# Optimization experiments

Measured on AMD Instinct MI355X. Metric: run time of the kernel, lower is better.

## Reference

```python
import jax, jax.numpy as jnp
import numpy as np

L1, L2, B = 512, 512, 2
D1, D2, BN = 256, 256, 256
NEG = jnp.float32(-1e12)


def setup_inputs() -> dict:
    key = jax.random.key(0)
    ks = jax.random.split(key, 8)
    s = 0.05
    return {
        "ctx_1": jax.random.normal(ks[0], (L1, B, D1), jnp.float32),
        "ctx_2": jax.random.normal(ks[1], (L2, B, D2), jnp.float32),
        "ctx_1_mask": jnp.ones((L1, B), jnp.float32),
        "ctx_2_mask": jnp.ones((L2, B), jnp.float32),
        # mlp_hid: Conv2d(D1+D2 -> BN, 1x1) with bias
        "Wh": jax.random.normal(ks[2], (D1 + D2, BN), jnp.float32) * s,
        "bh": jnp.zeros((BN,), jnp.float32),
        # mlp_out: Conv2d(BN -> 1, 1x1), bias=False (mlp_bias default)
        "wo": jax.random.normal(ks[3], (BN,), jnp.float32) * s,
        # project_1_to_2 / project_2_to_1: Linear(D1+D2 -> BN) with bias
        "W12": jax.random.normal(ks[4], (D2 + D1, BN), jnp.float32) * s,
        "b12": jnp.zeros((BN,), jnp.float32),
        "W21": jax.random.normal(ks[5], (D1 + D2, BN), jnp.float32) * s,
        "b21": jnp.zeros((BN,), jnp.float32),
    }


def reference(ctx_1, ctx_2, ctx_1_mask, ctx_2_mask, Wh, bh, wo, W12, b12, W21, b21):
    d1 = ctx_1.shape[-1]
    # 1x1 conv on cat([b_ctx_1, b_ctx_2]) == sum of two independent projections
    Wh1, Wh2 = Wh[:d1], Wh[d1:]
    p1 = jnp.einsum('lbd,dk->blk', ctx_1, Wh1)            # (B, L1, K)
    p2 = jnp.einsum('mbd,dk->bmk', ctx_2, Wh2)            # (B, L2, K)
    hidden = jnp.tanh(p1[:, :, None, :] + p2[:, None, :, :] + bh)  # (B, L1, L2, K)
    affinity = jnp.einsum('blmk,k->blm', hidden, wo)      # (B, L1, L2)
    # masked in both directions
    affinity = affinity + (1.0 - ctx_1_mask.T)[:, :, None] * NEG
    affinity = affinity + (1.0 - ctx_2_mask.T)[:, None, :] * NEG
    # 1 -> 2 direction: softmax over L2
    dist_1_to_2 = jax.nn.softmax(affinity, axis=2)        # (B, L1, L2)
    context_1_to_2 = jnp.einsum('lbd,blm->mbd', ctx_1, dist_1_to_2)  # (L2, B, D1)
    seq_1_to_2 = jnp.tanh(jnp.concatenate([ctx_2, context_1_to_2], axis=-1) @ W12 + b12)
    # 2 -> 1 direction: softmax over L1 (then contracted over L2, as in the torch code)
    dist_2_to_1 = jax.nn.softmax(affinity, axis=1)        # (B, L1, L2)
    context_2_to_1 = jnp.einsum('mbd,blm->lbd', ctx_2, dist_2_to_1)  # (L1, B, D2)
    seq_2_to_1 = jnp.tanh(jnp.concatenate([ctx_1, context_2_to_1], axis=-1) @ W21 + b21)
    return (seq_2_to_1, seq_1_to_2)
```

## Files before the change

### kernel.cpp

```cpp
#include <hip/hip_runtime.h>


#define NEGC (-1e12f)
#define TWO_LOG2E 2.8853900817779268f
#define LOG2E 1.4426950408889634f
#define N2LOG2E (-2.8853900817779268f)

typedef __attribute__((ext_vector_type(8))) short bf16x8;
typedef __attribute__((ext_vector_type(4))) float f32x4;

__device__ __forceinline__ short f2bf(float x)
{
    union { float f; unsigned u; } v; v.f = x;
    unsigned r = (v.u + 0x7FFFu + ((v.u >> 16) & 1u)) >> 16;
    return (short)r;
}

__global__ __launch_bounds__(256) void k_proj(
    const float* __restrict__ ctx1, const float* __restrict__ ctx2,
    const float* __restrict__ Wh, const float* __restrict__ bh,
    const float* __restrict__ W12, const float* __restrict__ b12,
    const float* __restrict__ W21, const float* __restrict__ b21,
    const float* __restrict__ mask1, const float* __restrict__ mask2,
    float* __restrict__ E1, float* __restrict__ E2,
    float* __restrict__ P12, float* __restrict__ U1,
    float* __restrict__ P21, float* __restrict__ U2,
    float* __restrict__ p1, float* __restrict__ p2,
    float* __restrict__ S1, float* __restrict__ S2)
{
    const int t  = threadIdx.x;
    const int g  = blockIdx.z;
    const int r0 = blockIdx.x * 64;
    const int n0 = blockIdx.y * 64;

    const float* A; const float* W; const float* bias; int expm; float* outp;
    switch (g) {
      case 0:  A=ctx1; W=Wh;        bias=bh;   expm=1; outp=E1;  break;
      case 1:  A=ctx2; W=Wh+65536;  bias=0;    expm=1; outp=E2;  break;
      case 2:  A=ctx2; W=W12;       bias=b12;  expm=0; outp=P12; break;
      case 3:  A=ctx1; W=W12+65536; bias=0;    expm=0; outp=U1;  break;
      case 4:  A=ctx1; W=W21;       bias=b21;  expm=0; outp=P21; break;
      default: A=ctx2; W=W21+65536; bias=0;    expm=0; outp=U2;  break;
    }

    if (g == 0 && blockIdx.x == 0 && blockIdx.y == 0) {
        for (int idx = t; idx < 1024; idx += 256) {
            int row = idx >> 1, b = idx & 1;
            p1[b * 512 + row] = __builtin_amdgcn_exp2f(LOG2E * (1.f - mask1[idx]) * NEGC);
            p2[b * 512 + row] = __builtin_amdgcn_exp2f(LOG2E * (1.f - mask2[idx]) * NEGC);
            S1[b * 512 + row] = 0.f;
            S2[b * 512 + row] = 0.f;
        }
    }

    __shared__ __align__(16) short Abf[64 * 136];
    __shared__ __align__(16) short Bbf[64 * 136];

    const int w    = t >> 6;
    const int lane = t & 63;
    const int quad = lane >> 4;
    const int lr   = lane & 15;

    f32x4 acc[4] = {};

    for (int kc = 0; kc < 256; kc += 128) {
        #pragma unroll
        for (int i = 0; i < 8; ++i) {
            int slot = i * 256 + t;
            int r = slot >> 5, kq = (slot & 31) << 2;
            float4 v = *(const float4*)(A + (r0 + r) * 256 + kc + kq);
            short4 s; s.x = f2bf(v.x); s.y = f2bf(v.y); s.z = f2bf(v.z); s.w = f2bf(v.w);
            *(short4*)(Abf + r * 136 + kq) = s;
        }
        #pragma unroll
        for (int i = 0; i < 8; ++i) {
            int slot = i * 256 + t;
            int bk = slot >> 4, bn4 = (slot & 15) << 2;
            float4 v = *(const float4*)(W + (kc + bk) * 256 + n0 + bn4);
            Bbf[(bn4 + 0) * 136 + bk] = f2bf(v.x);
            Bbf[(bn4 + 1) * 136 + bk] = f2bf(v.y);
            Bbf[(bn4 + 2) * 136 + bk] = f2bf(v.z);
            Bbf[(bn4 + 3) * 136 + bk] = f2bf(v.w);
        }
        __syncthreads();
        #pragma unroll
        for (int s = 0; s < 4; ++s) {
            const int kb = s * 32 + quad * 8;
            bf16x8 a = *(const bf16x8*)(Abf + (w * 16 + lr) * 136 + kb);
            #pragma unroll
            for (int nc = 0; nc < 4; ++nc) {
                bf16x8 b = *(const bf16x8*)(Bbf + (nc * 16 + lr) * 136 + kb);
                acc[nc] = __builtin_amdgcn_mfma_f32_16x16x32_bf16(a, b, acc[nc], 0, 0, 0);
            }
        }
        __syncthreads();
    }

    #pragma unroll
    for (int nc = 0; nc < 4; ++nc) {
        const int col = n0 + nc * 16 + lr;
        const float bv = bias ? bias[col] : 0.f;
        #pragma unroll
        for (int reg = 0; reg < 4; ++reg) {
            int row  = r0 + w * 16 + quad * 4 + reg;
            int orow = ((row & 1) << 9) + (row >> 1);
            float v = acc[nc][reg] + bv;
            if (expm) v = __builtin_amdgcn_exp2f(v * TWO_LOG2E);
            outp[orow * 256 + col] = v;
        }
    }
}

#define PAIR(AV, QV, WV, ACC) do {                                    \
    float x0_ = fmaf(AV.x, QV.x, 1.f);                                \
    float x1_ = fmaf(AV.y, QV.y, 1.f);                                \
    float x2_ = fmaf(AV.z, QV.z, 1.f);                                \
    float x3_ = fmaf(AV.w, QV.w, 1.f);                                \
    float r01_ = __builtin_amdgcn_rcpf(x0_ * x1_);                    \
    float r23_ = __builtin_amdgcn_rcpf(x2_ * x3_);                    \
    float z01_ = fmaf(WV.y, x0_, WV.x * x1_);                         \
    float z23_ = fmaf(WV.w, x2_, WV.z * x3_);                         \
    ACC = fmaf(r01_, z01_, ACC);                                      \
    ACC = fmaf(r23_, z23_, ACC);                                      \
} while (0)

__global__ __launch_bounds__(256) void k_aff(
    const float* __restrict__ E1g, const float* __restrict__ E2g,
    const float* __restrict__ wo,
    const float* __restrict__ p1g, const float* __restrict__ p2g,
    float* __restrict__ EN, float* __restrict__ ET,
    float* __restrict__ S1, float* __restrict__ S2)
{
    const int t  = threadIdx.x;
    const int l0 = blockIdx.x * 32, m0 = blockIdx.y * 32, b = blockIdx.z;

    __shared__ __align__(16) float E2s[32 * 132];
    __shared__ __align__(16) float affs[32 * 36];

    const int tl = t >> 4, tm = t & 15;
    const float* e1a = E1g + (((b << 9) + l0 + tl) << 8);
    const float* e1b = E1g + (((b << 9) + l0 + tl + 16) << 8);
    float acc[2][2] = {};

    for (int kc = 0; kc < 256; kc += 128) {
        #pragma unroll
        for (int i = 0; i < 4; ++i) {
            int slot = i * 256 + t;
            int r = slot >> 5, kq = (slot & 31) << 2;
            *(float4*)(E2s + r * 132 + kq) =
                *(const float4*)(E2g + (((b << 9) + m0 + r) << 8) + kc + kq);
        }
        __syncthreads();
        #pragma unroll 4
        for (int k0 = 0; k0 < 128; k0 += 4) {
            const float4 w  = *(const float4*)(wo + kc + k0);
            const float4 a0 = *(const float4*)(e1a + kc + k0);
            const float4 a1 = *(const float4*)(e1b + kc + k0);
            const float4 q0 = *(const float4*)(E2s + tm * 132 + k0);
            const float4 q1 = *(const float4*)(E2s + (tm + 16) * 132 + k0);
            PAIR(a0, q0, w, acc[0][0]);
            PAIR(a0, q1, w, acc[0][1]);
            PAIR(a1, q0, w, acc[1][0]);
            PAIR(a1, q1, w, acc[1][1]);
        }
        __syncthreads();
    }

    affs[tl * 36 + tm]             = __builtin_amdgcn_exp2f(acc[0][0] * N2LOG2E);
    affs[tl * 36 + tm + 16]        = __builtin_amdgcn_exp2f(acc[0][1] * N2LOG2E);
    affs[(tl + 16) * 36 + tm]      = __builtin_amdgcn_exp2f(acc[1][0] * N2LOG2E);
    affs[(tl + 16) * 36 + tm + 16] = __builtin_amdgcn_exp2f(acc[1][1] * N2LOG2E);
    __syncthreads();

    const int r  = t >> 3;
    const int c4 = (t & 7) << 2;
    {
        float4 e = *(const float4*)(affs + r * 36 + c4);
        const float p1r = p1g[(b << 9) + l0 + r];
        float4 vn = make_float4(e.x * p1r, e.y * p1r, e.z * p1r, e.w * p1r);
        *(float4*)(EN + (((b << 9) + l0 + r) << 9) + m0 + c4) = vn;
        float4 p2v = *(const float4*)(p2g + (b << 9) + m0 + c4);
        float s = (e.x * p2v.x + e.y * p2v.y) + (e.z * p2v.z + e.w * p2v.w);
        s += __shfl_xor(s, 1, 64);
        s += __shfl_xor(s, 2, 64);
        s += __shfl_xor(s, 4, 64);
        if ((t & 7) == 0) atomicAdd(S1 + (b << 9) + l0 + r, s);
    }
    {
        float4 te;
        te.x = affs[(c4 + 0) * 36 + r];
        te.y = affs[(c4 + 1) * 36 + r];
        te.z = affs[(c4 + 2) * 36 + r];
        te.w = affs[(c4 + 3) * 36 + r];
        const float p2r = p2g[(b << 9) + m0 + r];
        float4 vt = make_float4(te.x * p2r, te.y * p2r, te.z * p2r, te.w * p2r);
        *(float4*)(ET + (((b << 9) + m0 + r) << 9) + l0 + c4) = vt;
        float4 p1v = *(const float4*)(p1g + (b << 9) + l0 + c4);
        float s = (te.x * p1v.x + te.y * p1v.y) + (te.z * p1v.z + te.w * p1v.w);
        s += __shfl_xor(s, 1, 64);
        s += __shfl_xor(s, 2, 64);
        s += __shfl_xor(s, 4, 64);
        if ((t & 7) == 0) atomicAdd(S2 + (b << 9) + m0 + r, s);
    }
}

__global__ __launch_bounds__(256) void k_final(
    const float* __restrict__ EN, const float* __restrict__ ET,
    const float* __restrict__ U1, const float* __restrict__ U2,
    const float* __restrict__ P12, const float* __restrict__ P21,
    const float* __restrict__ S1, const float* __restrict__ S2,
    float* __restrict__ out)
{
    const int t   = threadIdx.x;
    const int r0  = blockIdx.x * 32, n0 = blockIdx.y * 32;
    const int dir = blockIdx.z >> 1, b = blockIdx.z & 1;
    const float* Ag = (dir == 0 ? ET  : EN)  + b * 262144;
    const float* Sg = (dir == 0 ? S1  : S2)  + b * 512;
    const float* Bg = (dir == 0 ? U1  : U2)  + b * 131072;
    const float* Pg = (dir == 0 ? P12 : P21) + b * 131072;
    float* o = out + (dir == 0 ? 262144 : 0);

    __shared__ __align__(16) short Abf[32 * 72];
    __shared__ __align__(16) short Bbf[32 * 72];
    __shared__ __align__(16) float rs[512];

    for (int i = t; i < 512; i += 256)
        rs[i] = __builtin_amdgcn_rcpf(Sg[i]);
    __syncthreads();

    const int w    = t >> 6;
    const int lane = t & 63;
    const int quad = lane >> 4;
    const int lr   = lane & 15;
    const int wr   = (w >> 1) << 4, wc = (w & 1) << 4;
    f32x4 acc = {};

    for (int kc = 0; kc < 512; kc += 64) {
        #pragma unroll
        for (int i = 0; i < 2; ++i) {
            int slot = i * 256 + t;
            int r = slot >> 4, kq = (slot & 15) << 2;
            float4 v = *(const float4*)(Ag + ((r0 + r) << 9) + kc + kq);
            const float* rp = rs + kc + kq;
            short4 s;
            s.x = f2bf(v.x * rp[0]); s.y = f2bf(v.y * rp[1]);
            s.z = f2bf(v.z * rp[2]); s.w = f2bf(v.w * rp[3]);
            *(short4*)(Abf + r * 72 + kq) = s;
        }
        #pragma unroll
        for (int i = 0; i < 2; ++i) {
            int slot = i * 256 + t;
            int bk = slot >> 3, bn4 = (slot & 7) << 2;
            float4 v = *(const float4*)(Bg + ((kc + bk) << 8) + n0 + bn4);
            Bbf[(bn4 + 0) * 72 + bk] = f2bf(v.x);
            Bbf[(bn4 + 1) * 72 + bk] = f2bf(v.y);
            Bbf[(bn4 + 2) * 72 + bk] = f2bf(v.z);
            Bbf[(bn4 + 3) * 72 + bk] = f2bf(v.w);
        }
        __syncthreads();
        #pragma unroll
        for (int s = 0; s < 2; ++s) {
            const int kb = s * 32 + quad * 8;
            bf16x8 a = *(const bf16x8*)(Abf + (wr + lr) * 72 + kb);
            bf16x8 bb = *(const bf16x8*)(Bbf + (wc + lr) * 72 + kb);
            acc = __builtin_amdgcn_mfma_f32_16x16x32_bf16(a, bb, acc, 0, 0, 0);
        }
        __syncthreads();
    }

    const int col = n0 + wc + lr;
    #pragma unroll
    for (int reg = 0; reg < 4; ++reg) {
        const int m = r0 + wr + quad * 4 + reg;
        float v = acc[reg] + Pg[(m << 8) + col];
        float tv = 1.f - 2.f * __builtin_amdgcn_rcpf(
                       __builtin_amdgcn_exp2f(v * TWO_LOG2E) + 1.f);
        o[((m << 1) + b) * 256 + col] = tv;
    }
}

extern "C" void kernel_launch(void* const* d_in, const int* in_sizes, int n_in,
                              void* d_out, int out_size, void* d_ws, size_t ws_size,
                              hipStream_t stream)
{
    const float* ctx1 = (const float*)d_in[0];
    const float* ctx2 = (const float*)d_in[1];
    const float* m1   = (const float*)d_in[2];
    const float* m2   = (const float*)d_in[3];
    const float* Wh   = (const float*)d_in[4];
    const float* bh   = (const float*)d_in[5];
    const float* wo   = (const float*)d_in[6];
    const float* W12  = (const float*)d_in[7];
    const float* b12  = (const float*)d_in[8];
    const float* W21  = (const float*)d_in[9];
    const float* b21  = (const float*)d_in[10];
    float* out = (float*)d_out;
    float* ws  = (float*)d_ws;

    float* E1  = ws;
    float* E2  = E1  + 262144;
    float* P12 = E2  + 262144;
    float* U1  = P12 + 262144;
    float* P21 = U1  + 262144;
    float* U2  = P21 + 262144;
    float* p1  = U2  + 262144;
    float* p2  = p1  + 1024;
    float* S1  = p2  + 1024;
    float* S2  = S1  + 1024;
    float* EN  = S2  + 1024;
    float* ET  = EN  + 524288;

    hipLaunchKernelGGL(k_proj, dim3(16, 4, 6), dim3(256), 0, stream,
                       ctx1, ctx2, Wh, bh, W12, b12, W21, b21, m1, m2,
                       E1, E2, P12, U1, P21, U2, p1, p2, S1, S2);
    hipLaunchKernelGGL(k_aff, dim3(16, 16, 2), dim3(256), 0, stream,
                       E1, E2, wo, p1, p2, EN, ET, S1, S2);
    hipLaunchKernelGGL(k_final, dim3(16, 8, 4), dim3(256), 0, stream,
                       EN, ET, U1, U2, P12, P21, S1, S2, out);
}
```

Before: 119.4 us.

## Store affinity intermediates as bf16 and fold softmax scale into B operand

k_aff now writes the EN/ET intermediates as bf16 instead of fp32, which halves their write traffic and the read traffic in k_final. k_final moves the reciprocal softmax-denominator scaling from the A rows onto the B operand (indexed by k). It stages the whole 512-deep B tile in shared memory once and then reads A fragments directly from global memory into MFMA, with no per-chunk staging or barriers. The risks are uncoalesced 16-byte direct global reads of A, a larger shared-memory footprint, and rounding to bf16 before normalization.

```diff
diff --git a/kernel.cpp b/kernel.cpp
--- a/kernel.cpp
+++ b/kernel.cpp
@@ -128,7 +128,7 @@
     const float* __restrict__ E1g, const float* __restrict__ E2g,
     const float* __restrict__ wo,
     const float* __restrict__ p1g, const float* __restrict__ p2g,
-    float* __restrict__ EN, float* __restrict__ ET,
+    short* __restrict__ ENb, short* __restrict__ ETb,
     float* __restrict__ S1, float* __restrict__ S2)
 {
     const int t  = threadIdx.x;
@@ -177,8 +177,10 @@
     {
         float4 e = *(const float4*)(affs + r * 36 + c4);
         const float p1r = p1g[(b << 9) + l0 + r];
-        float4 vn = make_float4(e.x * p1r, e.y * p1r, e.z * p1r, e.w * p1r);
-        *(float4*)(EN + (((b << 9) + l0 + r) << 9) + m0 + c4) = vn;
+        short4 sv;
+        sv.x = f2bf(e.x * p1r); sv.y = f2bf(e.y * p1r);
+        sv.z = f2bf(e.z * p1r); sv.w = f2bf(e.w * p1r);
+        *(short4*)(ENb + (((b << 9) + l0 + r) << 9) + m0 + c4) = sv;
         float4 p2v = *(const float4*)(p2g + (b << 9) + m0 + c4);
         float s = (e.x * p2v.x + e.y * p2v.y) + (e.z * p2v.z + e.w * p2v.w);
         s += __shfl_xor(s, 1, 64);
@@ -193,8 +195,10 @@
         te.z = affs[(c4 + 2) * 36 + r];
         te.w = affs[(c4 + 3) * 36 + r];
         const float p2r = p2g[(b << 9) + m0 + r];
-        float4 vt = make_float4(te.x * p2r, te.y * p2r, te.z * p2r, te.w * p2r);
-        *(float4*)(ET + (((b << 9) + m0 + r) << 9) + l0 + c4) = vt;
+        short4 sv;
+        sv.x = f2bf(te.x * p2r); sv.y = f2bf(te.y * p2r);
+        sv.z = f2bf(te.z * p2r); sv.w = f2bf(te.w * p2r);
+        *(short4*)(ETb + (((b << 9) + m0 + r) << 9) + l0 + c4) = sv;
         float4 p1v = *(const float4*)(p1g + (b << 9) + l0 + c4);
         float s = (te.x * p1v.x + te.y * p1v.y) + (te.z * p1v.z + te.w * p1v.w);
         s += __shfl_xor(s, 1, 64);
@@ -205,7 +209,7 @@
 }
 
 __global__ __launch_bounds__(256) void k_final(
-    const float* __restrict__ EN, const float* __restrict__ ET,
+    const short* __restrict__ ENb, const short* __restrict__ ETb,
     const float* __restrict__ U1, const float* __restrict__ U2,
     const float* __restrict__ P12, const float* __restrict__ P21,
     const float* __restrict__ S1, const float* __restrict__ S2,
@@ -214,18 +218,30 @@
     const int t   = threadIdx.x;
     const int r0  = blockIdx.x * 32, n0 = blockIdx.y * 32;
     const int dir = blockIdx.z >> 1, b = blockIdx.z & 1;
-    const float* Ag = (dir == 0 ? ET  : EN)  + b * 262144;
+    const short* Ag = (dir == 0 ? ETb : ENb) + b * 262144;
     const float* Sg = (dir == 0 ? S1  : S2)  + b * 512;
     const float* Bg = (dir == 0 ? U1  : U2)  + b * 131072;
     const float* Pg = (dir == 0 ? P12 : P21) + b * 131072;
     float* o = out + (dir == 0 ? 262144 : 0);
 
-    __shared__ __align__(16) short Abf[32 * 72];
-    __shared__ __align__(16) short Bbf[32 * 72];
+    __shared__ __align__(16) short Bbf[32 * 520];
     __shared__ __align__(16) float rs[512];
 
     for (int i = t; i < 512; i += 256)
         rs[i] = __builtin_amdgcn_rcpf(Sg[i]);
+    __syncthreads();
+
+    #pragma unroll
+    for (int i = 0; i < 16; ++i) {
+        int slot = i * 256 + t;
+        int bk = slot >> 3, bn4 = (slot & 7) << 2;
+        float4 v = *(const float4*)(Bg + (bk << 8) + n0 + bn4);
+        const float r_ = rs[bk];
+        Bbf[(bn4 + 0) * 520 + bk] = f2bf(v.x * r_);
+        Bbf[(bn4 + 1) * 520 + bk] = f2bf(v.y * r_);
+        Bbf[(bn4 + 2) * 520 + bk] = f2bf(v.z * r_);
+        Bbf[(bn4 + 3) * 520 + bk] = f2bf(v.w * r_);
+    }
     __syncthreads();
 
     const int w    = t >> 6;
@@ -233,39 +249,15 @@
     const int quad = lane >> 4;
     const int lr   = lane & 15;
     const int wr   = (w >> 1) << 4, wc = (w & 1) << 4;
+    const short* ap = Ag + (r0 + wr + lr) * 512;
     f32x4 acc = {};
 
-    for (int kc = 0; kc < 512; kc += 64) {
-        #pragma unroll
-        for (int i = 0; i < 2; ++i) {
-            int slot = i * 256 + t;
-            int r = slot >> 4, kq = (slot & 15) << 2;
-            float4 v = *(const float4*)(Ag + ((r0 + r) << 9) + kc + kq);
-            const float* rp = rs + kc + kq;
-            short4 s;
-            s.x = f2bf(v.x * rp[0]); s.y = f2bf(v.y * rp[1]);
-            s.z = f2bf(v.z * rp[2]); s.w = f2bf(v.w * rp[3]);
-            *(short4*)(Abf + r * 72 + kq) = s;
-        }
-        #pragma unroll
-        for (int i = 0; i < 2; ++i) {
-            int slot = i * 256 + t;
-            int bk = slot >> 3, bn4 = (slot & 7) << 2;
-            float4 v = *(const float4*)(Bg + ((kc + bk) << 8) + n0 + bn4);
-            Bbf[(bn4 + 0) * 72 + bk] = f2bf(v.x);
-            Bbf[(bn4 + 1) * 72 + bk] = f2bf(v.y);
-            Bbf[(bn4 + 2) * 72 + bk] = f2bf(v.z);
-            Bbf[(bn4 + 3) * 72 + bk] = f2bf(v.w);
-        }
-        __syncthreads();
-        #pragma unroll
-        for (int s = 0; s < 2; ++s) {
-            const int kb = s * 32 + quad * 8;
-            bf16x8 a = *(const bf16x8*)(Abf + (wr + lr) * 72 + kb);
-            bf16x8 bb = *(const bf16x8*)(Bbf + (wc + lr) * 72 + kb);
-            acc = __builtin_amdgcn_mfma_f32_16x16x32_bf16(a, bb, acc, 0, 0, 0);
-        }
-        __syncthreads();
+    #pragma unroll
+    for (int s = 0; s < 16; ++s) {
+        const int kb = s * 32 + quad * 8;
+        bf16x8 a  = *(const bf16x8*)(ap + kb);
+        bf16x8 bb = *(const bf16x8*)(Bbf + (wc + lr) * 520 + kb);
+        acc = __builtin_amdgcn_mfma_f32_16x16x32_bf16(a, bb, acc, 0, 0, 0);
     }
 
     const int col = n0 + wc + lr;
@@ -307,14 +299,14 @@
     float* p2  = p1  + 1024;
     float* S1  = p2  + 1024;
     float* S2  = S1  + 1024;
-    float* EN  = S2  + 1024;
-    float* ET  = EN  + 524288;
+    short* ENb = (short*)(S2 + 1024);
+    short* ETb = ENb + 524288;
 
     hipLaunchKernelGGL(k_proj, dim3(16, 4, 6), dim3(256), 0, stream,
                        ctx1, ctx2, Wh, bh, W12, b12, W21, b21, m1, m2,
                        E1, E2, P12, U1, P21, U2, p1, p2, S1, S2);
     hipLaunchKernelGGL(k_aff, dim3(16, 16, 2), dim3(256), 0, stream,
-                       E1, E2, wo, p1, p2, EN, ET, S1, S2);
+                       E1, E2, wo, p1, p2, ENb, ETb, S1, S2);
     hipLaunchKernelGGL(k_final, dim3(16, 8, 4), dim3(256), 0, stream,
-                       EN, ET, U1, U2, P12, P21, S1, S2, out);
-}
+                       ENb, ETb, U1, U2, P12, P21, S1, S2, out);
+}
```

Measured after the change: 119.1 us. About the same (-0.3%).
